# Performance work log

Measured on AMD Instinct MI355X. Metric: run time of the kernel, lower is better.

## Reference

```python
import jax, jax.numpy as jnp
import numpy as np

TOP_K = 2
BALANCE_W = 0.01


def setup_inputs() -> dict:
    key = jax.random.key(0)
    ks = jax.random.split(key, 9)
    B, T, D, E, H, S = 4, 2048, 1024, 16, 1024, 2

    def w(k, shape):
        return jax.random.normal(k, shape, jnp.float32) * 0.02

    return {
        "x": jax.random.normal(ks[0], (B, T, D), jnp.float32),
        "router_w": w(ks[1], (D, E)),
        "router_bias": jnp.zeros((E,), jnp.float32),
        "Wg": w(ks[2], (E, D, H)),
        "Wu": w(ks[3], (E, D, H)),
        "Wd": w(ks[4], (E, H, D)),
        "sWg": w(ks[5], (D, S * H)),
        "sWu": w(ks[6], (D, S * H)),
        "sWd": w(ks[7], (S * H, D)),
    }


def reference(x, router_w, router_bias, Wg, Wu, Wd, sWg, sWu, sWd):
    B, T, D = x.shape
    E = router_w.shape[1]
    flat = x.reshape(-1, D)                      # [N, D], N = B*T
    N = flat.shape[0]

    # ---- router (fp32, matching x.float() in torch ref) ----
    logits = flat @ router_w                     # [N, E]
    probs = jax.nn.softmax(logits, axis=-1)      # unbiased probs
    _, indices = jax.lax.top_k(logits + router_bias, TOP_K)  # [N, K]
    weights = jnp.take_along_axis(probs, indices, axis=-1)   # [N, K]
    weights = weights / jnp.maximum(weights.sum(-1, keepdims=True), 1e-9)

    # per-(token, expert) combine weight; top-k indices are unique per row
    C = jnp.zeros((N, E), flat.dtype).at[jnp.arange(N)[:, None], indices].add(weights)
    expert_load = jax.nn.one_hot(indices, E, dtype=jnp.float32).sum((0, 1))  # [E]

    # ---- routed SwiGLU experts: scan over experts, masked combine ----
    def body(acc, per_e):
        wg, wu, wd, c = per_e                    # [D,H],[D,H],[H,D],[N]
        h = jax.nn.silu(flat @ wg) * (flat @ wu) # [N, H]
        return acc + (h @ wd) * c[:, None], None

    routed, _ = jax.lax.scan(body, jnp.zeros_like(flat), (Wg, Wu, Wd, C.T))

    # ---- shared expert ----
    shared = (jax.nn.silu(flat @ sWg) * (flat @ sWu)) @ sWd

    out = (routed + shared).reshape(B, T, D)

    # ---- Switch/DeepSeek balance loss (training mode) ----
    expert_fraction = expert_load / (N * TOP_K)
    probability_fraction = probs.mean(0)
    balance = BALANCE_W * E * jnp.sum(expert_fraction * probability_fraction)

    return out, balance, expert_load
```

## Files before the change

### kernel.cpp

```cpp
#include <hip/hip_runtime.h>
#include <stdint.h>

#define N_TOK 8192
#define DDIM  1024
#define NEXP  16
#define HDIM  1024
#define SHDIM 2048
#define TM 128
#define BK 64
#define MT_R 144

#define SH_GU_NT  32
#define SH_GU_WGS 2048
#define RT_GU_NT  16
#define RT_GU_WGS 2304
#define GU_WGS    4352
#define GU_SLOTS  (GU_WGS / 8)
#define TR2_WGS   4608
#define TR2_SLOTS (TR2_WGS / 8)
#define GUF_WGS   (GU_WGS + TR2_WGS)

#define TND 128
#define DN_WGS    2176

#define RT_WGS    512
#define TR1_WGS   9216
#define RTF_WGS   (RT_WGS + TR1_WGS)

#define CPAD 16

typedef __bf16 bf16x8 __attribute__((ext_vector_type(8)));
typedef float  f32x4  __attribute__((ext_vector_type(4)));

__device__ __forceinline__ unsigned short f2bf(float f) {
  union { float f; unsigned u; } v; v.f = f;
  unsigned r = v.u + 0x7fffu + ((v.u >> 16) & 1u);
  return (unsigned short)(r >> 16);
}
__device__ __forceinline__ float bf2f(unsigned short u) {
  union { unsigned u; float f; } v; v.u = (unsigned)u << 16; return v.f;
}

__device__ __forceinline__ void gload16(const void* g, void* l) {
  __builtin_amdgcn_global_load_lds(
      (const __attribute__((address_space(1))) void*)g,
      (__attribute__((address_space(3))) void*)l, 16, 0, 0);
}

__device__ __forceinline__ int xcd_swizzle() {
  int nwg = (int)gridDim.x;
  int b = (int)blockIdx.x;
  return (b & 7) * (nwg >> 3) + (b >> 3);
}

__device__ __forceinline__ bool seg_lookup(const int* __restrict__ cnt, int tm,
                                           int& e, int& segStart, int& segCnt) {
  int o = 0; e = 0; segStart = 0; segCnt = 0;
#pragma unroll
  for (int i = 0; i < NEXP; i++) {
    int c = cnt[i * CPAD];
    if (tm >= o) { e = i; segStart = o; segCnt = c; }
    o += (c + 127) & ~127;
  }
  return tm < o;
}


__device__ __forceinline__ void do_transpose64(
    const float* __restrict__ src, unsigned short* __restrict__ dst,
    int R, int C, int tc, int tr, float* tile ) {
  int rx = threadIdx.x >> 4;
  int cx = (threadIdx.x & 15) * 4;
#pragma unroll
  for (int p = 0; p < 4; p++) {
    int r = p * 16 + rx;
    float4 v = *(const float4*)(src + (size_t)(tr + r) * C + tc + cx);
    tile[(cx + 0) * 65 + r] = v.x;
    tile[(cx + 1) * 65 + r] = v.y;
    tile[(cx + 2) * 65 + r] = v.z;
    tile[(cx + 3) * 65 + r] = v.w;
  }
  __syncthreads();
#pragma unroll
  for (int p = 0; p < 4; p++) {
    int c = p * 16 + rx;
    float v0 = tile[c * 65 + cx + 0];
    float v1 = tile[c * 65 + cx + 1];
    float v2 = tile[c * 65 + cx + 2];
    float v3 = tile[c * 65 + cx + 3];
    ushort4 o; o.x = f2bf(v0); o.y = f2bf(v1); o.z = f2bf(v2); o.w = f2bf(v3);
    *(ushort4*)(dst + (size_t)(tc + c) * R + tr + cx) = o;
  }
}


__global__ void k_zero(int* cnt, int* cursor, float* probsum) {
  int t = threadIdx.x;
  if (t < NEXP * CPAD) { cnt[t] = 0; cursor[t] = 0; probsum[t] = 0.f; }
}

__global__ __launch_bounds__(256) void k_router_tr(
    const float* __restrict__ x, const float* __restrict__ rw,
    const float* __restrict__ rb, int* __restrict__ cnt,
    int* __restrict__ tok_idx, float* __restrict__ tok_w,
    float* __restrict__ probsum, unsigned short* __restrict__ Xbf,
    const float* __restrict__ Wg, const float* __restrict__ Wu,
    const float* __restrict__ sWg, const float* __restrict__ sWu,
    unsigned short* __restrict__ WgT, unsigned short* __restrict__ WuT,
    unsigned short* __restrict__ sWgT, unsigned short* __restrict__ sWuT) {
  __shared__ __attribute__((aligned(16))) float smem[NEXP * 1024 + NEXP];
  const int t = threadIdx.x;

  if (blockIdx.x >= RT_WGS) {
    int id = blockIdx.x - RT_WGS;
    float* tile = smem;
    if (id < 4096) {
      int mat = id >> 8, tl = id & 255;
      do_transpose64(Wg + ((size_t)mat << 20), WgT + ((size_t)mat << 20),
                     1024, 1024, (tl & 15) * 64, (tl >> 4) * 64, tile);
    } else if (id < 8192) {
      int mat = (id - 4096) >> 8, tl = id & 255;
      do_transpose64(Wu + ((size_t)mat << 20), WuT + ((size_t)mat << 20),
                     1024, 1024, (tl & 15) * 64, (tl >> 4) * 64, tile);
    } else if (id < 8704) {
      int tl = id - 8192;
      do_transpose64(sWg, sWgT, 1024, 2048, (tl & 31) * 64, (tl >> 5) * 64, tile);
    } else {
      int tl = id - 8704;
      do_transpose64(sWu, sWuT, 1024, 2048, (tl & 31) * 64, (tl >> 5) * 64, tile);
    }
    return;
  }

  float* rwT = smem;
  float* ps  = smem + NEXP * 1024;
  if (t < NEXP) ps[t] = 0.f;
  {
    int dbase = t >> 2, e0 = (t & 3) * 4;
#pragma unroll
    for (int c = 0; c < 16; c++) {
      int d = dbase + 64 * c;
      float4 v = *(const float4*)(rw + (size_t)d * NEXP + e0);
      rwT[(e0 + 0) * 1024 + d] = v.x;
      rwT[(e0 + 1) * 1024 + d] = v.y;
      rwT[(e0 + 2) * 1024 + d] = v.z;
      rwT[(e0 + 3) * 1024 + d] = v.w;
    }
  }
  __syncthreads();
  const int lane = t & 63, wv = t >> 6;
  const int tok0 = blockIdx.x * 16 + wv * 4;
  float acc[4][NEXP];
#pragma unroll
  for (int tt = 0; tt < 4; tt++)
#pragma unroll
    for (int e = 0; e < NEXP; e++) acc[tt][e] = 0.f;

#pragma unroll
  for (int c = 0; c < 4; c++) {
    int d = lane * 4 + 256 * c;
    float4 xv[4];
#pragma unroll
    for (int tt = 0; tt < 4; tt++) {
      xv[tt] = *(const float4*)(x + (size_t)(tok0 + tt) * DDIM + d);
      ushort4 o;
      o.x = f2bf(xv[tt].x); o.y = f2bf(xv[tt].y);
      o.z = f2bf(xv[tt].z); o.w = f2bf(xv[tt].w);
      *(ushort4*)(Xbf + (size_t)(tok0 + tt) * DDIM + d) = o;
    }
#pragma unroll
    for (int e = 0; e < NEXP; e++) {
      float4 w4 = *(const float4*)(&rwT[e * 1024 + d]);
#pragma unroll
      for (int tt = 0; tt < 4; tt++) {
        acc[tt][e] = fmaf(xv[tt].x, w4.x, acc[tt][e]);
        acc[tt][e] = fmaf(xv[tt].y, w4.y, acc[tt][e]);
        acc[tt][e] = fmaf(xv[tt].z, w4.z, acc[tt][e]);
        acc[tt][e] = fmaf(xv[tt].w, w4.w, acc[tt][e]);
      }
    }
  }
#pragma unroll
  for (int tt = 0; tt < 4; tt++)
#pragma unroll
    for (int e = 0; e < NEXP; e++) {
      float v = acc[tt][e];
#pragma unroll
      for (int o = 32; o; o >>= 1) v += __shfl_xor(v, o);
      acc[tt][e] = v;
    }

#pragma unroll
  for (int tt = 0; tt < 4; tt++) {
    if (lane == tt) {
      int tok = tok0 + tt;
      float mx = acc[tt][0];
#pragma unroll
      for (int e = 1; e < NEXP; e++) mx = fmaxf(mx, acc[tt][e]);
      float p[NEXP]; float s = 0.f;
#pragma unroll
      for (int e = 0; e < NEXP; e++) { p[e] = __expf(acc[tt][e] - mx); s += p[e]; }
      float inv = 1.f / s;
#pragma unroll
      for (int e = 0; e < NEXP; e++) { p[e] *= inv; atomicAdd(&ps[e], p[e]); }
      int i0 = 0; float b0 = acc[tt][0] + rb[0];
#pragma unroll
      for (int e = 1; e < NEXP; e++) { float v = acc[tt][e] + rb[e]; if (v > b0) { b0 = v; i0 = e; } }
      int i1 = -1; float b1 = -3.4e38f;
#pragma unroll
      for (int e = 0; e < NEXP; e++) {
        if (e == i0) continue;
        float v = acc[tt][e] + rb[e]; if (v > b1) { b1 = v; i1 = e; }
      }
      float w0 = 0.f, w1 = 0.f;
#pragma unroll
      for (int e = 0; e < NEXP; e++) { if (e == i0) w0 = p[e]; if (e == i1) w1 = p[e]; }
      float ssum = fmaxf(w0 + w1, 1e-9f);
      w0 /= ssum; w1 /= ssum;
      atomicAdd(&cnt[i0 * CPAD], 1); atomicAdd(&cnt[i1 * CPAD], 1);
      tok_idx[tok * 2]     = i0; tok_idx[tok * 2 + 1] = i1;
      tok_w[tok * 2]       = w0; tok_w[tok * 2 + 1]   = w1;
    }
  }
  __syncthreads();
  if (t < NEXP) atomicAdd(&probsum[t * CPAD], ps[t]);
}

__global__ __launch_bounds__(256) void k_assign(
    const int* __restrict__ tok_idx, int* __restrict__ cursor,
    const int* __restrict__ cnt, int* __restrict__ row_token,
    int* __restrict__ tok_rows) {
  int i = blockIdx.x * 256 + threadIdx.x;
  int e = tok_idx[i];
  int o = 0, myoff = 0;
#pragma unroll
  for (int k = 0; k < NEXP; k++) {
    if (e == k) myoff = o;
    o += (cnt[k * CPAD] + 127) & ~127;
  }
  int pos = atomicAdd(&cursor[e * CPAD], 1);
  int row = myoff + pos;
  row_token[row] = i >> 1;
  tok_rows[i] = row;
}


__global__ __launch_bounds__(256, 4) void k_gateup_all(
    const unsigned short* __restrict__ Xbf,
    const unsigned short* __restrict__ sWgT,
    const unsigned short* __restrict__ sWuT,
    const unsigned short* __restrict__ WgT,
    const unsigned short* __restrict__ WuT,
    unsigned short* __restrict__ Hs,
    unsigned short* __restrict__ Hr,
    const int* __restrict__ cnt,
    const int* __restrict__ row_token,
    const float* __restrict__ Wd, const float* __restrict__ sWd,
    unsigned short* __restrict__ WdT, unsigned short* __restrict__ sWdT) {
  __shared__ __attribute__((aligned(16))) char smem[32768];
  unsigned short* As  = (unsigned short*)smem;
  unsigned short* Bgs = (unsigned short*)(smem + 16384);
  unsigned short* Bus = (unsigned short*)(smem + 24576);

  const int slot = blockIdx.x >> 3;
  const int xcd  = blockIdx.x & 7;

  if (slot >= GU_SLOTS) {
    int tid = xcd * TR2_SLOTS + (slot - GU_SLOTS);
    float* tile = (float*)smem;
    if (tid < 4096) {
      int mat = tid >> 8, tl = tid & 255;
      do_transpose64(Wd + ((size_t)mat << 20), WdT + ((size_t)mat << 20),
                     1024, 1024, (tl & 15) * 64, (tl >> 4) * 64, tile);
    } else {
      int tl = tid - 4096;
      do_transpose64(sWd, sWdT, 2048, 1024, (tl & 15) * 64, (tl >> 4) * 64, tile);
    }
    return;
  }

  const int wg = xcd * GU_SLOTS + slot;
  const int t = threadIdx.x;
  const int lane = t & 63, wv = t >> 6;
  const int lr  = lane >> 3;
  const int kbx = (lane & 7) ^ lr;

  int tm, tn, validEnd, Nh;
  const unsigned short *Bgp, *Bup;
  unsigned short* Hout;
  const unsigned short* pA[4];

  if (wg < SH_GU_WGS) {
    int band = wg >> 9;
    int r = wg & 511;
    tm = (r >> 3) * TM;
    tn = (band * 8 + (r & 7)) * 64;
    validEnd = 0x7fffffff;
    Bgp = sWgT; Bup = sWuT;
    Hout = Hs; Nh = SHDIM;
#pragma unroll
    for (int j = 0; j < 4; j++)
      pA[j] = Xbf + (size_t)(tm + (wv * 4 + j) * 8 + lr) * DDIM;
  } else {
    int u = wg - SH_GU_WGS;
    int band = u / 1152;
    int r = u % 1152;
    tm = (r >> 3) * TM;
    tn = (band * 8 + (r & 7)) * 64;
    int e, segStart, segCnt;
    if (!seg_lookup(cnt, tm, e, segStart, segCnt)) return;
    validEnd = segStart + segCnt;
    if (tm >= validEnd) return;
    Bgp = WgT + (size_t)e * HDIM * DDIM;
    Bup = WuT + (size_t)e * HDIM * DDIM;
    Hout = Hr; Nh = HDIM;
#pragma unroll
    for (int j = 0; j < 4; j++) {
      int row = tm + (wv * 4 + j) * 8 + lr;
      int tok = row < validEnd ? row_token[row] : 0;
      pA[j] = Xbf + (size_t)tok * DDIM;
    }
  }
  const unsigned short* pBg[2];
  const unsigned short* pBu[2];
#pragma unroll
  for (int j = 0; j < 2; j++) {
    int row = tn + (wv * 2 + j) * 8 + lr;
    pBg[j] = Bgp + (size_t)row * DDIM;
    pBu[j] = Bup + (size_t)row * DDIM;
  }

  auto stage = [&](int k0) {
#pragma unroll
    for (int j = 0; j < 4; j++)
      gload16(pA[j] + k0 + kbx * 8, (void*)&As[(wv * 4 + j) * 512]);
#pragma unroll
    for (int j = 0; j < 2; j++) {
      gload16(pBg[j] + k0 + kbx * 8, (void*)&Bgs[(wv * 2 + j) * 512]);
      gload16(pBu[j] + k0 + kbx * 8, (void*)&Bus[(wv * 2 + j) * 512]);
    }
  };

  f32x4 accG[4][2] = {};
  f32x4 accU[4][2] = {};
  const int wr = wv >> 1, wc = wv & 1;
  const int rbase = lane & 15;
  const int kgrp = lane >> 4;

  for (int k0 = 0; k0 < DDIM; k0 += BK) {
    if (k0) __syncthreads();
    stage(k0);
    __syncthreads();
#pragma unroll
    for (int kk = 0; kk < 2; kk++) {
      bf16x8 af[4], gf[2], uf[2];
      int kbl = kk * 4 + kgrp;
#pragma unroll
      for (int i = 0; i < 4; i++) {
        int r = wr * 64 + i * 16 + rbase;
        af[i] = *(const bf16x8*)((const char*)As + r * 128 + ((kbl ^ (r & 7)) << 4));
      }
#pragma unroll
      for (int j = 0; j < 2; j++) {
        int r = wc * 32 + j * 16 + rbase;
        gf[j] = *(const bf16x8*)((const char*)Bgs + r * 128 + ((kbl ^ (r & 7)) << 4));
        uf[j] = *(const bf16x8*)((const char*)Bus + r * 128 + ((kbl ^ (r & 7)) << 4));
      }
#pragma unroll
      for (int i = 0; i < 4; i++)
#pragma unroll
        for (int j = 0; j < 2; j++) {
          accG[i][j] = __builtin_amdgcn_mfma_f32_16x16x32_bf16(af[i], gf[j], accG[i][j], 0, 0, 0);
          accU[i][j] = __builtin_amdgcn_mfma_f32_16x16x32_bf16(af[i], uf[j], accU[i][j], 0, 0, 0);
        }
    }
  }

  const int orow0 = tm + wr * 64 + (lane >> 4) * 4;
  const int ocol0 = tn + wc * 32 + (lane & 15);
#pragma unroll
  for (int i = 0; i < 4; i++)
#pragma unroll
    for (int j = 0; j < 2; j++)
#pragma unroll
      for (int r = 0; r < 4; r++) {
        int row = orow0 + i * 16 + r;
        if (row < validEnd) {
          float g = accG[i][j][r], u = accU[i][j][r];
          float h = g / (1.f + __expf(-g)) * u;
          Hout[(size_t)row * Nh + ocol0 + j * 16] = f2bf(h);
        }
      }
}

__global__ __launch_bounds__(256, 4) void k_down_all(
    const unsigned short* __restrict__ Hs,
    const unsigned short* __restrict__ Hr,
    const unsigned short* __restrict__ sWdT,
    const unsigned short* __restrict__ WdT,
    float* __restrict__ out,
    float* __restrict__ Pbuf,
    unsigned short* __restrict__ Rbuf,
    const int* __restrict__ cnt) {
  __shared__ unsigned short As[TM * BK];
  __shared__ unsigned short Bs[TND * BK];

  const int wg = xcd_swizzle();
  const int t = threadIdx.x;
  const int lane = t & 63, wv = t >> 6;
  const int lr  = lane >> 3;
  const int kbx = (lane & 7) ^ lr;

  int tm, tn, validEnd;
  bool routed;
  float* outF = out;
  const unsigned short* pA[4];
  const unsigned short* pB[4];

  if (wg < 1024) {
    routed = false;
    int half = wg >> 9;
    int r = wg & 511;
    tm = (r >> 3) * TM;
    tn = (r & 7) * TND;
    validEnd = 0x7fffffff;
    outF = half ? Pbuf : out;
    int kbase = half << 10;
#pragma unroll
    for (int j = 0; j < 4; j++) {
      pA[j] = Hs + (size_t)(tm + (wv * 4 + j) * 8 + lr) * SHDIM + kbase;
      pB[j] = sWdT + (size_t)(tn + (wv * 4 + j) * 8 + lr) * SHDIM + kbase;
    }
  } else {
    routed = true;
    int wgr = wg - 1024;
    tm = (wgr >> 3) * TM;
    tn = (wgr & 7) * TND;
    int e, segStart, segCnt;
    if (!seg_lookup(cnt, tm, e, segStart, segCnt)) return;
    validEnd = segStart + segCnt;
    if (tm >= validEnd) return;
    const unsigned short* B = WdT + (size_t)e * DDIM * HDIM;
#pragma unroll
    for (int j = 0; j < 4; j++) {
      pA[j] = Hr + (size_t)(tm + (wv * 4 + j) * 8 + lr) * HDIM;
      pB[j] = B + (size_t)(tn + (wv * 4 + j) * 8 + lr) * HDIM;
    }
  }

  auto stage = [&](int k0) {
#pragma unroll
    for (int j = 0; j < 4; j++) {
      gload16(pA[j] + k0 + kbx * 8, (void*)&As[(wv * 4 + j) * 512]);
      gload16(pB[j] + k0 + kbx * 8, (void*)&Bs[(wv * 4 + j) * 512]);
    }
  };

  f32x4 acc[4][4] = {};
  const int wr = wv >> 1, wc = wv & 1;
  const int rbase = lane & 15;
  const int kgrp = lane >> 4;

  for (int k0 = 0; k0 < 1024; k0 += BK) {
    if (k0) __syncthreads();
    stage(k0);
    __syncthreads();
#pragma unroll
    for (int kk = 0; kk < 2; kk++) {
      bf16x8 af[4], bf[4];
      int kbl = kk * 4 + kgrp;
#pragma unroll
      for (int i = 0; i < 4; i++) {
        int r = wr * 64 + i * 16 + rbase;
        af[i] = *(const bf16x8*)((const char*)&As[0] + r * 128 + ((kbl ^ (r & 7)) << 4));
      }
#pragma unroll
      for (int j = 0; j < 4; j++) {
        int r = wc * 64 + j * 16 + rbase;
        bf[j] = *(const bf16x8*)((const char*)&Bs[0] + r * 128 + ((kbl ^ (r & 7)) << 4));
      }
#pragma unroll
      for (int i = 0; i < 4; i++)
#pragma unroll
        for (int j = 0; j < 4; j++)
          acc[i][j] = __builtin_amdgcn_mfma_f32_16x16x32_bf16(af[i], bf[j], acc[i][j], 0, 0, 0);
    }
  }

  const int orow0 = tm + wr * 64 + (lane >> 4) * 4;
  const int ocol0 = tn + wc * 64 + (lane & 15);
#pragma unroll
  for (int i = 0; i < 4; i++)
#pragma unroll
    for (int j = 0; j < 4; j++)
#pragma unroll
      for (int r = 0; r < 4; r++) {
        int row = orow0 + i * 16 + r;
        int col = ocol0 + j * 16;
        if (routed) {
          if (row < validEnd) Rbuf[(size_t)row * DDIM + col] = f2bf(acc[i][j][r]);
        } else {
          outF[(size_t)row * DDIM + col] = acc[i][j][r];
        }
      }
}

__global__ __launch_bounds__(256) void k_combine(
    float* __restrict__ out, const float* __restrict__ Pbuf,
    const unsigned short* __restrict__ Rbuf,
    const int* __restrict__ tok_rows, const float* __restrict__ tok_w,
    const float* __restrict__ probsum, const int* __restrict__ cnt,
    float* __restrict__ out_tail) {
  int tok = blockIdx.x;
  int c = threadIdx.x;
  int r0 = tok_rows[tok * 2], r1 = tok_rows[tok * 2 + 1];
  float w0 = tok_w[tok * 2],  w1 = tok_w[tok * 2 + 1];
  float4 o  = ((const float4*)(out + (size_t)tok * DDIM))[c];
  float4 p  = ((const float4*)(Pbuf + (size_t)tok * DDIM))[c];
  ushort4 a = ((const ushort4*)(Rbuf + (size_t)r0 * DDIM))[c];
  ushort4 b = ((const ushort4*)(Rbuf + (size_t)r1 * DDIM))[c];
  o.x += p.x + w0 * bf2f(a.x) + w1 * bf2f(b.x);
  o.y += p.y + w0 * bf2f(a.y) + w1 * bf2f(b.y);
  o.z += p.z + w0 * bf2f(a.z) + w1 * bf2f(b.z);
  o.w += p.w + w0 * bf2f(a.w) + w1 * bf2f(b.w);
  ((float4*)(out + (size_t)tok * DDIM))[c] = o;

  if (blockIdx.x == 0) {
    if (threadIdx.x == 0) {
      float bal = 0.f;
      for (int e = 0; e < NEXP; e++) {
        float frac = (float)cnt[e * CPAD] / (float)(N_TOK * 2);
        bal += frac * (probsum[e * CPAD] / (float)N_TOK);
      }
      out_tail[0] = 0.01f * (float)NEXP * bal;
    }
    if (threadIdx.x < NEXP) out_tail[1 + threadIdx.x] = (float)cnt[threadIdx.x * CPAD];
  }
}


extern "C" void kernel_launch(void* const* d_in, const int* in_sizes, int n_in,
                              void* d_out, int out_size, void* d_ws, size_t ws_size,
                              hipStream_t stream) {
  const float* x   = (const float*)d_in[0];
  const float* rw  = (const float*)d_in[1];
  const float* rb  = (const float*)d_in[2];
  const float* Wg  = (const float*)d_in[3];
  const float* Wu  = (const float*)d_in[4];
  const float* Wd  = (const float*)d_in[5];
  const float* sWg = (const float*)d_in[6];
  const float* sWu = (const float*)d_in[7];
  const float* sWd = (const float*)d_in[8];
  float* out = (float*)d_out;

  uint8_t* w = (uint8_t*)d_ws;
  size_t off = 0;
  auto alloc = [&](size_t bytes) -> void* {
    void* p = w + off;
    off += (bytes + 255) & ~(size_t)255;
    return p;
  };

  int*   cnt      = (int*)alloc(NEXP * CPAD * 4);
  int*   cursor   = (int*)alloc(NEXP * CPAD * 4);
  float* probsum  = (float*)alloc(NEXP * CPAD * 4);
  int*   tok_idx  = (int*)alloc((size_t)N_TOK * 2 * 4);
  float* tok_w    = (float*)alloc((size_t)N_TOK * 2 * 4);
  int*   tok_rows = (int*)alloc((size_t)N_TOK * 2 * 4);
  int*   row_tok  = (int*)alloc((size_t)MT_R * TM * 4);
  unsigned short* Xbf  = (unsigned short*)alloc((size_t)N_TOK * DDIM * 2);
  unsigned short* Hs   = (unsigned short*)alloc((size_t)N_TOK * SHDIM * 2);
  unsigned short* Hr   = (unsigned short*)alloc((size_t)MT_R * TM * HDIM * 2);
  unsigned short* Rbuf = (unsigned short*)alloc((size_t)MT_R * TM * DDIM * 2);
  unsigned short* WgT  = (unsigned short*)alloc((size_t)NEXP * HDIM * DDIM * 2);
  unsigned short* WuT  = (unsigned short*)alloc((size_t)NEXP * HDIM * DDIM * 2);
  unsigned short* WdT  = (unsigned short*)alloc((size_t)NEXP * DDIM * HDIM * 2);
  unsigned short* sWgT = (unsigned short*)alloc((size_t)SHDIM * DDIM * 2);
  unsigned short* sWuT = (unsigned short*)alloc((size_t)SHDIM * DDIM * 2);
  unsigned short* sWdT = (unsigned short*)alloc((size_t)DDIM * SHDIM * 2);

  float* Pbuf = (float*)WgT;

  if (off > ws_size) return;

  k_zero<<<1, 256, 0, stream>>>(cnt, cursor, probsum);
  k_router_tr<<<RTF_WGS, 256, 0, stream>>>(
      x, rw, rb, cnt, tok_idx, tok_w, probsum, Xbf,
      Wg, Wu, sWg, sWu, WgT, WuT, sWgT, sWuT);
  k_assign<<<64, 256, 0, stream>>>(tok_idx, cursor, cnt, row_tok, tok_rows);
  k_gateup_all<<<GUF_WGS, 256, 0, stream>>>(
      Xbf, sWgT, sWuT, WgT, WuT, Hs, Hr, cnt, row_tok,
      Wd, sWd, WdT, sWdT);
  k_down_all<<<DN_WGS, 256, 0, stream>>>(
      Hs, Hr, sWdT, WdT, out, Pbuf, Rbuf, cnt);
  k_combine<<<N_TOK, 256, 0, stream>>>(
      out, Pbuf, Rbuf, tok_rows, tok_w, probsum, cnt, out + (size_t)N_TOK * DDIM);
}
```

Before: 395.4 us.

## Rewrite gate/up GEMM as 256x128 8-wave tiles with double-buffered LDS pipeline

```diff
diff --git a/kernel.cpp b/kernel.cpp
--- a/kernel.cpp
+++ b/kernel.cpp
@@ -8,24 +8,19 @@
 #define SHDIM 2048
 #define TM 128
 #define BK 64
-#define MT_R 144
-
-#define SH_GU_NT  32
-#define SH_GU_WGS 2048
-#define RT_GU_NT  16
-#define RT_GU_WGS 2304
-#define GU_WGS    4352
-#define GU_SLOTS  (GU_WGS / 8)
-#define TR2_WGS   4608
-#define TR2_SLOTS (TR2_WGS / 8)
-#define GUF_WGS   (GU_WGS + TR2_WGS)
+#define NT 16
+#define MAXROWS 20480
+
+#define GU8_WGS 1152
 
 #define TND 128
-#define DN_WGS    2176
-
-#define RT_WGS    512
-#define TR1_WGS   9216
-#define RTF_WGS   (RT_WGS + TR1_WGS)
+#define DN_WGS (1024 + 1280)
+
+#define RT_WGS  512
+#define TR1_WGS 9216
+#define RTF_WGS (RT_WGS + TR1_WGS)
+
+#define TRD_WGS (4096 + 512 + 64)
 
 #define CPAD 16
 
@@ -47,6 +42,11 @@
       (__attribute__((address_space(3))) void*)l, 16, 0, 0);
 }
 
+#define FENCE() asm volatile("" ::: "memory")
+#define SBAR()  do { FENCE(); __builtin_amdgcn_s_barrier(); FENCE(); } while (0)
+#define VMCNT(n) asm volatile("s_waitcnt vmcnt(" #n ")" ::: "memory")
+#define LGKM0()  asm volatile("s_waitcnt lgkmcnt(0)" ::: "memory")
+
 __device__ __forceinline__ int xcd_swizzle() {
   int nwg = (int)gridDim.x;
   int b = (int)blockIdx.x;
@@ -60,9 +60,15 @@
   for (int i = 0; i < NEXP; i++) {
     int c = cnt[i * CPAD];
     if (tm >= o) { e = i; segStart = o; segCnt = c; }
-    o += (c + 127) & ~127;
+    o += (c + 255) & ~255;
   }
   return tm < o;
+}
+
+
+__global__ void k_zero(int* cnt, int* cursor, float* probsum) {
+  int t = threadIdx.x;
+  if (t < NEXP * CPAD) { cnt[t] = 0; cursor[t] = 0; probsum[t] = 0.f; }
 }
 
 
@@ -91,12 +97,6 @@
     ushort4 o; o.x = f2bf(v0); o.y = f2bf(v1); o.z = f2bf(v2); o.w = f2bf(v3);
     *(ushort4*)(dst + (size_t)(tc + c) * R + tr + cx) = o;
   }
-}
-
-
-__global__ void k_zero(int* cnt, int* cursor, float* probsum) {
-  int t = threadIdx.x;
-  if (t < NEXP * CPAD) { cnt[t] = 0; cursor[t] = 0; probsum[t] = 0.f; }
 }
 
 __global__ __launch_bounds__(256) void k_router_tr(
@@ -226,26 +226,78 @@
   if (t < NEXP) atomicAdd(&probsum[t * CPAD], ps[t]);
 }
 
-__global__ __launch_bounds__(256) void k_assign(
+__global__ __launch_bounds__(256) void k_trd_assign(
+    const float* __restrict__ Wd, const float* __restrict__ sWd,
+    unsigned short* __restrict__ WdT, unsigned short* __restrict__ sWdT,
     const int* __restrict__ tok_idx, int* __restrict__ cursor,
     const int* __restrict__ cnt, int* __restrict__ row_token,
     int* __restrict__ tok_rows) {
-  int i = blockIdx.x * 256 + threadIdx.x;
-  int e = tok_idx[i];
-  int o = 0, myoff = 0;
-#pragma unroll
-  for (int k = 0; k < NEXP; k++) {
-    if (e == k) myoff = o;
-    o += (cnt[k * CPAD] + 127) & ~127;
-  }
-  int pos = atomicAdd(&cursor[e * CPAD], 1);
-  int row = myoff + pos;
-  row_token[row] = i >> 1;
-  tok_rows[i] = row;
-}
-
-
-__global__ __launch_bounds__(256, 4) void k_gateup_all(
+  __shared__ float tile[64 * 65];
+  int id = blockIdx.x;
+  if (id < 4096) {
+    int mat = id >> 8, tl = id & 255;
+    do_transpose64(Wd + ((size_t)mat << 20), WdT + ((size_t)mat << 20),
+                   1024, 1024, (tl & 15) * 64, (tl >> 4) * 64, tile);
+  } else if (id < 4608) {
+    int tl = id - 4096;
+    do_transpose64(sWd, sWdT, 2048, 1024, (tl & 15) * 64, (tl >> 4) * 64, tile);
+  } else {
+    int i = (id - 4608) * 256 + threadIdx.x;
+    int e = tok_idx[i];
+    int o = 0, myoff = 0;
+#pragma unroll
+    for (int k = 0; k < NEXP; k++) {
+      if (e == k) myoff = o;
+      o += (cnt[k * CPAD] + 255) & ~255;
+    }
+    int pos = atomicAdd(&cursor[e * CPAD], 1);
+    int row = myoff + pos;
+    row_token[row] = i >> 1;
+    tok_rows[i] = row;
+  }
+}
+
+
+#define ISSUE(tile, hk) do { \
+    gload16(pS[hk][0] + (size_t)(tile) * 64, (void*)&lds[(tile) & 1][hk][ldsb]);        \
+    gload16(pS[hk][1] + (size_t)(tile) * 64, (void*)&lds[(tile) & 1][hk][ldsb + 4096]); \
+  } while (0)
+
+#define PHASE(AH, BH, ACC, DOW, W, itile, ihk)                                  \
+  {                                                                             \
+    if (DOW) { if (t < NT - 2) { VMCNT(W); } else { VMCNT(0); } }               \
+    SBAR();                                                                     \
+    bf16x8 af[4][2], bv[2][2];                                                  \
+    const char* Ab = (const char*)&lds[cur][AH][0];                             \
+    const char* Bb = (const char*)&lds[cur][BH][0];                             \
+    _Pragma("unroll")                                                           \
+    for (int i = 0; i < 4; i++)                                                 \
+      _Pragma("unroll")                                                         \
+      for (int kk = 0; kk < 2; kk++)                                            \
+        af[i][kk] = *(const bf16x8*)(Ab + (wr * 64 + i * 16 + rb) * 128 +       \
+                                     ((kk * 64 + kq) ^ sx));                    \
+    _Pragma("unroll")                                                           \
+    for (int j = 0; j < 2; j++)                                                 \
+      _Pragma("unroll")                                                         \
+      for (int kk = 0; kk < 2; kk++)                                            \
+        bv[j][kk] = *(const bf16x8*)(Bb + (wc * 32 + j * 16 + rb) * 128 +       \
+                                     ((kk * 64 + kq) ^ sx));                    \
+    if ((itile) < NT) { ISSUE(itile, ihk); }                                    \
+    __builtin_amdgcn_s_setprio(1);                                              \
+    _Pragma("unroll")                                                           \
+    for (int i = 0; i < 4; i++)                                                 \
+      _Pragma("unroll")                                                         \
+      for (int j = 0; j < 2; j++)                                               \
+        _Pragma("unroll")                                                       \
+        for (int kk = 0; kk < 2; kk++)                                          \
+          ACC[i][j] = __builtin_amdgcn_mfma_f32_16x16x32_bf16(                  \
+              af[i][kk], bv[j][kk], ACC[i][j], 0, 0, 0);                        \
+    __builtin_amdgcn_s_setprio(0);                                              \
+    LGKM0();                                                                    \
+    __builtin_amdgcn_sched_barrier(0);                                          \
+  }
+
+__global__ __launch_bounds__(512, 2) void k_gateup8(
     const unsigned short* __restrict__ Xbf,
     const unsigned short* __restrict__ sWgT,
     const unsigned short* __restrict__ sWuT,
@@ -254,144 +306,101 @@
     unsigned short* __restrict__ Hs,
     unsigned short* __restrict__ Hr,
     const int* __restrict__ cnt,
-    const int* __restrict__ row_token,
-    const float* __restrict__ Wd, const float* __restrict__ sWd,
-    unsigned short* __restrict__ WdT, unsigned short* __restrict__ sWdT) {
-  __shared__ __attribute__((aligned(16))) char smem[32768];
-  unsigned short* As  = (unsigned short*)smem;
-  unsigned short* Bgs = (unsigned short*)(smem + 16384);
-  unsigned short* Bus = (unsigned short*)(smem + 24576);
-
-  const int slot = blockIdx.x >> 3;
-  const int xcd  = blockIdx.x & 7;
-
-  if (slot >= GU_SLOTS) {
-    int tid = xcd * TR2_SLOTS + (slot - GU_SLOTS);
-    float* tile = (float*)smem;
-    if (tid < 4096) {
-      int mat = tid >> 8, tl = tid & 255;
-      do_transpose64(Wd + ((size_t)mat << 20), WdT + ((size_t)mat << 20),
-                     1024, 1024, (tl & 15) * 64, (tl >> 4) * 64, tile);
-    } else {
-      int tl = tid - 4096;
-      do_transpose64(sWd, sWdT, 2048, 1024, (tl & 15) * 64, (tl >> 4) * 64, tile);
-    }
-    return;
-  }
-
-  const int wg = xcd * GU_SLOTS + slot;
-  const int t = threadIdx.x;
-  const int lane = t & 63, wv = t >> 6;
-  const int lr  = lane >> 3;
-  const int kbx = (lane & 7) ^ lr;
+    const int* __restrict__ row_token) {
+  __shared__ __attribute__((aligned(16))) unsigned short lds[2][4][8192];
+
+  const int wg = xcd_swizzle();
+  const int T = threadIdx.x;
+  const int lane = T & 63, w = T >> 6;
+  const int wr = w >> 2, wc = w & 3;
 
   int tm, tn, validEnd, Nh;
-  const unsigned short *Bgp, *Bup;
+  const unsigned short *Bg, *Bu;
   unsigned short* Hout;
-  const unsigned short* pA[4];
-
-  if (wg < SH_GU_WGS) {
-    int band = wg >> 9;
-    int r = wg & 511;
-    tm = (r >> 3) * TM;
-    tn = (band * 8 + (r & 7)) * 64;
+  bool routed;
+
+  if (wg < 512) {
+    routed = false;
+    int band = wg >> 8, r = wg & 255;
+    tm = (r >> 3) * 256;
+    tn = (band * 8 + (r & 7)) * 128;
     validEnd = 0x7fffffff;
-    Bgp = sWgT; Bup = sWuT;
-    Hout = Hs; Nh = SHDIM;
-#pragma unroll
-    for (int j = 0; j < 4; j++)
-      pA[j] = Xbf + (size_t)(tm + (wv * 4 + j) * 8 + lr) * DDIM;
+    Bg = sWgT; Bu = sWuT; Hout = Hs; Nh = SHDIM;
   } else {
-    int u = wg - SH_GU_WGS;
-    int band = u / 1152;
-    int r = u % 1152;
-    tm = (r >> 3) * TM;
-    tn = (band * 8 + (r & 7)) * 64;
+    routed = true;
+    int u = wg - 512;
+    tm = (u >> 3) * 256;
+    tn = (u & 7) * 128;
     int e, segStart, segCnt;
     if (!seg_lookup(cnt, tm, e, segStart, segCnt)) return;
     validEnd = segStart + segCnt;
     if (tm >= validEnd) return;
-    Bgp = WgT + (size_t)e * HDIM * DDIM;
-    Bup = WuT + (size_t)e * HDIM * DDIM;
+    Bg = WgT + (size_t)e * HDIM * DDIM;
+    Bu = WuT + (size_t)e * HDIM * DDIM;
     Hout = Hr; Nh = HDIM;
-#pragma unroll
-    for (int j = 0; j < 4; j++) {
-      int row = tm + (wv * 4 + j) * 8 + lr;
-      int tok = row < validEnd ? row_token[row] : 0;
-      pA[j] = Xbf + (size_t)tok * DDIM;
-    }
-  }
-  const unsigned short* pBg[2];
-  const unsigned short* pBu[2];
-#pragma unroll
-  for (int j = 0; j < 2; j++) {
-    int row = tn + (wv * 2 + j) * 8 + lr;
-    pBg[j] = Bgp + (size_t)row * DDIM;
-    pBu[j] = Bup + (size_t)row * DDIM;
-  }
-
-  auto stage = [&](int k0) {
-#pragma unroll
-    for (int j = 0; j < 4; j++)
-      gload16(pA[j] + k0 + kbx * 8, (void*)&As[(wv * 4 + j) * 512]);
-#pragma unroll
-    for (int j = 0; j < 2; j++) {
-      gload16(pBg[j] + k0 + kbx * 8, (void*)&Bgs[(wv * 2 + j) * 512]);
-      gload16(pBu[j] + k0 + kbx * 8, (void*)&Bus[(wv * 2 + j) * 512]);
-    }
-  };
-
-  f32x4 accG[4][2] = {};
-  f32x4 accU[4][2] = {};
-  const int wr = wv >> 1, wc = wv & 1;
-  const int rbase = lane & 15;
-  const int kgrp = lane >> 4;
-
-  for (int k0 = 0; k0 < DDIM; k0 += BK) {
-    if (k0) __syncthreads();
-    stage(k0);
-    __syncthreads();
-#pragma unroll
-    for (int kk = 0; kk < 2; kk++) {
-      bf16x8 af[4], gf[2], uf[2];
-      int kbl = kk * 4 + kgrp;
-#pragma unroll
-      for (int i = 0; i < 4; i++) {
-        int r = wr * 64 + i * 16 + rbase;
-        af[i] = *(const bf16x8*)((const char*)As + r * 128 + ((kbl ^ (r & 7)) << 4));
-      }
-#pragma unroll
-      for (int j = 0; j < 2; j++) {
-        int r = wc * 32 + j * 16 + rbase;
-        gf[j] = *(const bf16x8*)((const char*)Bgs + r * 128 + ((kbl ^ (r & 7)) << 4));
-        uf[j] = *(const bf16x8*)((const char*)Bus + r * 128 + ((kbl ^ (r & 7)) << 4));
-      }
-#pragma unroll
-      for (int i = 0; i < 4; i++)
-#pragma unroll
-        for (int j = 0; j < 2; j++) {
-          accG[i][j] = __builtin_amdgcn_mfma_f32_16x16x32_bf16(af[i], gf[j], accG[i][j], 0, 0, 0);
-          accU[i][j] = __builtin_amdgcn_mfma_f32_16x16x32_bf16(af[i], uf[j], accU[i][j], 0, 0, 0);
+  }
+
+  const int srow = T >> 3;
+  const int colel = (((T & 7) ^ ((T >> 4) & 7)) << 3);
+  const unsigned short* pS[4][2];
+#pragma unroll
+  for (int R = 0; R < 2; R++) {
+    int r0 = tm + R * 64 + srow;
+    int r1 = tm + 128 + R * 64 + srow;
+    if (routed) {
+      int t0 = r0 < validEnd ? row_token[r0] : 0;
+      int t1 = r1 < validEnd ? row_token[r1] : 0;
+      pS[0][R] = Xbf + (size_t)t0 * DDIM + colel;
+      pS[1][R] = Xbf + (size_t)t1 * DDIM + colel;
+    } else {
+      pS[0][R] = Xbf + (size_t)r0 * DDIM + colel;
+      pS[1][R] = Xbf + (size_t)r1 * DDIM + colel;
+    }
+    pS[2][R] = Bg + (size_t)(tn + R * 64 + srow) * DDIM + colel;
+    pS[3][R] = Bu + (size_t)(tn + R * 64 + srow) * DDIM + colel;
+  }
+  const int ldsb = w * 512;
+
+  const int rb = lane & 15;
+  const int kq = (lane >> 4) * 16;
+  const int sx = (lane & 14) << 3;
+
+  f32x4 aG0[4][2] = {}, aG1[4][2] = {}, aU1[4][2] = {}, aU0[4][2] = {};
+
+  ISSUE(0, 2); ISSUE(0, 1); ISSUE(0, 0); ISSUE(0, 3); ISSUE(1, 2); ISSUE(1, 1);
+
+  for (int t = 0; t < NT; t++) {
+    const int cur = t & 1;
+    PHASE(0, 2, aG0, 1, 6, t + 1, 0)
+    PHASE(1, 2, aG1, 0, 0, t + 1, 3)
+    PHASE(1, 3, aU1, 1, 8, t + 2, 2)
+    PHASE(0, 3, aU0, 0, 0, t + 2, 1)
+  }
+
+  const int oc0 = tn + wc * 32 + rb;
+  const int or0 = tm + wr * 64 + (lane >> 4) * 4;
+#pragma unroll
+  for (int i = 0; i < 4; i++)
+#pragma unroll
+    for (int j = 0; j < 2; j++)
+#pragma unroll
+      for (int r = 0; r < 4; r++) {
+        int row0 = or0 + i * 16 + r;
+        int row1 = row0 + 128;
+        int col = oc0 + j * 16;
+        if (row0 < validEnd) {
+          float g = aG0[i][j][r], u = aU0[i][j][r];
+          Hout[(size_t)row0 * Nh + col] = f2bf(g / (1.f + __expf(-g)) * u);
         }
-    }
-  }
-
-  const int orow0 = tm + wr * 64 + (lane >> 4) * 4;
-  const int ocol0 = tn + wc * 32 + (lane & 15);
-#pragma unroll
-  for (int i = 0; i < 4; i++)
-#pragma unroll
-    for (int j = 0; j < 2; j++)
-#pragma unroll
-      for (int r = 0; r < 4; r++) {
-        int row = orow0 + i * 16 + r;
-        if (row < validEnd) {
-          float g = accG[i][j][r], u = accU[i][j][r];
-          float h = g / (1.f + __expf(-g)) * u;
-          Hout[(size_t)row * Nh + ocol0 + j * 16] = f2bf(h);
+        if (row1 < validEnd) {
+          float g = aG1[i][j][r], u = aU1[i][j][r];
+          Hout[(size_t)row1 * Nh + col] = f2bf(g / (1.f + __expf(-g)) * u);
         }
       }
 }
+
+
+__device__ __forceinline__ void gload16b(const void* g, void* l) { gload16(g, l); }
 
 __global__ __launch_bounds__(256, 4) void k_down_all(
     const unsigned short* __restrict__ Hs,
@@ -451,8 +460,8 @@
   auto stage = [&](int k0) {
 #pragma unroll
     for (int j = 0; j < 4; j++) {
-      gload16(pA[j] + k0 + kbx * 8, (void*)&As[(wv * 4 + j) * 512]);
-      gload16(pB[j] + k0 + kbx * 8, (void*)&Bs[(wv * 4 + j) * 512]);
+      gload16b(pA[j] + k0 + kbx * 8, (void*)&As[(wv * 4 + j) * 512]);
+      gload16b(pB[j] + k0 + kbx * 8, (void*)&Bs[(wv * 4 + j) * 512]);
     }
   };
 
@@ -567,19 +576,19 @@
   int*   tok_idx  = (int*)alloc((size_t)N_TOK * 2 * 4);
   float* tok_w    = (float*)alloc((size_t)N_TOK * 2 * 4);
   int*   tok_rows = (int*)alloc((size_t)N_TOK * 2 * 4);
-  int*   row_tok  = (int*)alloc((size_t)MT_R * TM * 4);
+  int*   row_tok  = (int*)alloc((size_t)MAXROWS * 4);
   unsigned short* Xbf  = (unsigned short*)alloc((size_t)N_TOK * DDIM * 2);
   unsigned short* Hs   = (unsigned short*)alloc((size_t)N_TOK * SHDIM * 2);
-  unsigned short* Hr   = (unsigned short*)alloc((size_t)MT_R * TM * HDIM * 2);
-  unsigned short* Rbuf = (unsigned short*)alloc((size_t)MT_R * TM * DDIM * 2);
+  unsigned short* Hr   = (unsigned short*)alloc((size_t)MAXROWS * DDIM * 2);
   unsigned short* WgT  = (unsigned short*)alloc((size_t)NEXP * HDIM * DDIM * 2);
   unsigned short* WuT  = (unsigned short*)alloc((size_t)NEXP * HDIM * DDIM * 2);
-  unsigned short* WdT  = (unsigned short*)alloc((size_t)NEXP * DDIM * HDIM * 2);
   unsigned short* sWgT = (unsigned short*)alloc((size_t)SHDIM * DDIM * 2);
   unsigned short* sWuT = (unsigned short*)alloc((size_t)SHDIM * DDIM * 2);
+  unsigned short* WdT  = (unsigned short*)alloc((size_t)NEXP * DDIM * HDIM * 2);
   unsigned short* sWdT = (unsigned short*)alloc((size_t)DDIM * SHDIM * 2);
 
   float* Pbuf = (float*)WgT;
+  unsigned short* Rbuf = WuT;
 
   if (off > ws_size) return;
 
@@ -587,10 +596,10 @@
   k_router_tr<<<RTF_WGS, 256, 0, stream>>>(
       x, rw, rb, cnt, tok_idx, tok_w, probsum, Xbf,
       Wg, Wu, sWg, sWu, WgT, WuT, sWgT, sWuT);
-  k_assign<<<64, 256, 0, stream>>>(tok_idx, cursor, cnt, row_tok, tok_rows);
-  k_gateup_all<<<GUF_WGS, 256, 0, stream>>>(
-      Xbf, sWgT, sWuT, WgT, WuT, Hs, Hr, cnt, row_tok,
-      Wd, sWd, WdT, sWdT);
+  k_trd_assign<<<TRD_WGS, 256, 0, stream>>>(
+      Wd, sWd, WdT, sWdT, tok_idx, cursor, cnt, row_tok, tok_rows);
+  k_gateup8<<<GU8_WGS, 512, 0, stream>>>(
+      Xbf, sWgT, sWuT, WgT, WuT, Hs, Hr, cnt, row_tok);
   k_down_all<<<DN_WGS, 256, 0, stream>>>(
       Hs, Hr, sWdT, WdT, out, Pbuf, Rbuf, cnt);
   k_combine<<<N_TOK, 256, 0, stream>>>(
```

Result: no change. 401.0 us (+1.4%).
